# Performance work log

Measured on AMD Instinct MI355X. Metric: run time of the kernel, lower is better.

Reference implementation:

```python
import jax, jax.numpy as jnp
import numpy as np

NZ, NX, NT, NS, NR = 150, 300, 1000, 4, 400
DX, DT, FREQ = 10.0, 0.001, 15.0
# 8th-order central-difference coefficients for the 2nd derivative
C = (-205.0 / 72.0, 8.0 / 5.0, -1.0 / 5.0, 8.0 / 315.0, -1.0 / 560.0)
HALO = 4


def setup_inputs() -> dict:
    key = jax.random.key(0)
    k1, k2 = jax.random.split(key, 2)
    # velocity model in [1500, 3500] m/s
    v_map = (1500.0 + 2000.0 * jax.random.uniform(k1, (NZ, NX))).astype(jnp.float32)
    # Ricker wavelet source, slightly perturbed per shot
    t = jnp.arange(NT, dtype=jnp.float32) * DT - 1.0 / FREQ
    a = (jnp.pi * FREQ * t) ** 2
    ricker = (1.0 - 2.0 * a) * jnp.exp(-a)
    s_amp = (ricker[None, :] * (1.0 + 0.01 * jax.random.normal(k2, (NS, NT)))).astype(jnp.float32)
    # sources: shallow depth, spread in x
    sz = jnp.full((NS,), 5, dtype=jnp.int32)
    sx = jnp.round(jnp.linspace(20, NX - 21, NS)).astype(jnp.int32)
    s_loc = jnp.stack([sz, sx], axis=-1)
    # receivers: near-surface line
    rz = jnp.full((NR,), 2, dtype=jnp.int32)
    rx = jnp.round(jnp.linspace(HALO, NX - 1 - HALO, NR)).astype(jnp.int32)
    r_loc = jnp.stack([rz, rx], axis=-1)
    return {"v_map": v_map, "s_amp": s_amp, "s_loc": s_loc, "r_loc": r_loc}


def _laplacian(u, nz, nx):
    # u: [S, nz, nx]; zero-padded 8th-order 5-point-per-axis stencil
    up = jnp.pad(u, ((0, 0), (HALO, HALO), (HALO, HALO)))
    out = 2.0 * C[0] * u
    for k in range(1, 5):
        out = out + C[k] * (
            up[:, HALO + k:HALO + k + nz, HALO:HALO + nx]
            + up[:, HALO - k:HALO - k + nz, HALO:HALO + nx]
            + up[:, HALO:HALO + nz, HALO + k:HALO + k + nx]
            + up[:, HALO:HALO + nz, HALO - k:HALO - k + nx]
        )
    return out / (DX * DX)


def reference(v_map, s_amp, s_loc, r_loc):
    nz, nx = v_map.shape
    ns = s_amp.shape[0]
    sz, sx = s_loc[:, 0], s_loc[:, 1]
    rz, rx = r_loc[:, 0], r_loc[:, 1]
    shot_ids = jnp.arange(ns)
    v2dt2 = (v_map * DT) ** 2                      # [nz, nx]
    src_scale = v2dt2[sz, sx]                      # [ns]

    def step(carry, amp_t):
        u_prev, u_cur = carry                      # each [ns, nz, nx]
        u_next = 2.0 * u_cur - u_prev + v2dt2[None] * _laplacian(u_cur, nz, nx)
        u_next = u_next.at[shot_ids, sz, sx].add(src_scale * amp_t)
        rec = u_next[:, rz, rx]                    # [ns, n_rec]
        return (u_cur, u_next), rec

    u0 = jnp.zeros((ns, nz, nx), dtype=v_map.dtype)
    _, recs = jax.lax.scan(step, (u0, u0), s_amp.T)  # recs: [nt, ns, n_rec]
    rec_gth = jnp.transpose(recs, (1, 0, 2))         # [ns, nt, n_rec]
    return rec_gth
```

## Files before the change

### kernel.cpp

```cpp
#include <hip/hip_runtime.h>


#define NZ_ 150
#define NX_ 300
#define NT_ 1000
#define NS_ 4
#define NR_ 400
#define KS_ 8
#define NCH_ 9
#define NBND_ 8
#define HW_ 32
#define ZW_ 168
#define LROWS_ 98
#define BUF_ (LROWS_*ZW_)
#define THR_ 512
#define NRND_ 125
#define HELE_ 4800
#define NBATCH 19

typedef float f4 __attribute__((ext_vector_type(4)));
typedef unsigned long long u64;

__device__ __forceinline__ void astore64(u64* p, u64 v) {
    __hip_atomic_store(p, v, __ATOMIC_RELAXED, __HIP_MEMORY_SCOPE_AGENT);
}
__device__ __forceinline__ int aload32(const int* p) {
    return __hip_atomic_load(p, __ATOMIC_RELAXED, __HIP_MEMORY_SCOPE_AGENT);
}
__device__ __forceinline__ void astore32(int* p, int v) {
    __hip_atomic_store(p, v, __ATOMIC_RELAXED, __HIP_MEMORY_SCOPE_AGENT);
}
__device__ __forceinline__ void ld2_issue(u64& d, const u64* p) {
    asm volatile("global_load_dwordx2 %0, %1, off sc0 sc1" : "=v"(d) : "v"(p));
}

__global__ __launch_bounds__(THR_) void wave_tb8b(
    const float* __restrict__ v_map, const float* __restrict__ s_amp,
    const int* __restrict__ s_loc, const int* __restrict__ r_loc,
    float* __restrict__ out, int* __restrict__ flags, u64* __restrict__ halo)
{
    extern __shared__ float smem[];
    const int bi = blockIdx.x;
    const int s = bi & 3;
    const int h = bi >> 2;
    const int tid = threadIdx.x;

    const int w  = 33 + (h < 3 ? 1 : 0);
    const int x0 = 33 * h + (h < 3 ? h : 3);
    const int rhi = HW_ + w;

    for (int i = tid; i < 2 * BUF_; i += THR_) smem[i] = 0.0f;

    const int zg = tid % 38;
    const int xp = tid / 38;
    const bool comp = (tid < 494);
    const int c0 = 4 + 4 * zg;
    const int rbase = 8 * xp;

    f4 v2r[8];
#pragma unroll
    for (int i = 0; i < 8; ++i) {
        f4 vv = {0.f, 0.f, 0.f, 0.f};
        const int row = rbase + i;
        const int x = x0 - HW_ + row;
        if (comp && x >= 0 && x < NX_) {
#pragma unroll
            for (int j = 0; j < 4; ++j) {
                const int z = min(4 * zg + j, NZ_ - 1);
                const float v = v_map[z * NX_ + x] * 0.001f;
                vv[j] = v * v * 0.01f;
            }
        }
        v2r[i] = vv;
    }

    const int sz = s_loc[2 * s], sx = s_loc[2 * s + 1];
    float sS = v_map[sz * NX_ + sx] * 0.001f; sS = sS * sS;
    const int srow = sx - x0 + HW_;
    const int szg = sz >> 2;
    const int scol = 4 + sz;

    bool rown = false; int rrow = 0, rcol = 0;
    if (tid < NR_) {
        const int rz = r_loc[2 * tid];
        const int rx = r_loc[2 * tid + 1];
        if (rx >= x0 && rx < x0 + w) { rown = true; rrow = HW_ + rx - x0; rcol = 4 + rz; }
    }

    __syncthreads();

    for (int r = 0; r < NRND_; ++r) {
        for (int k = 1; k <= KS_; ++k) {
            const int tau = KS_ * r + k;
            const int ext = 4 * (KS_ - k);
            const int L  = (h == 0)        ? HW_ : HW_ - ext;
            const int R  = (h == NCH_ - 1) ? rhi : rhi + ext;
            const float* cur = smem + ((tau + 1) & 1) * BUF_;
            float*       nxt = smem + (tau & 1) * BUF_;

            if (comp && rbase < R && rbase + 8 > L) {
                f4 W[9];
#pragma unroll
                for (int q = 0; q < 8; ++q) {
                    int rr = rbase - 4 + q; rr = rr < 0 ? 0 : rr;
                    W[q] = *(const f4*)&cur[rr * ZW_ + c0];
                }
#pragma unroll
                for (int i = 0; i < 8; ++i) {
                    const int row = rbase + i;
                    const int wr = (row + 4 < LROWS_) ? (row + 4) : (LROWS_ - 1);
                    W[8] = *(const f4*)&cur[wr * ZW_ + c0];
                    if (row >= L && row < R) {
                        const f4 lf = *(const f4*)&cur[row * ZW_ + c0 - 4];
                        const f4 rt = *(const f4*)&cur[row * ZW_ + c0 + 4];
                        const f4 pv = *(const f4*)&nxt[row * ZW_ + c0];
                        float xw[12];
#pragma unroll
                        for (int j = 0; j < 4; ++j) { xw[j] = lf[j]; xw[4 + j] = W[4][j]; xw[8 + j] = rt[j]; }
                        f4 res;
#pragma unroll
                        for (int j = 0; j < 4; ++j) {
                            const float ct = xw[4 + j];
                            float lap = 2.0f * (-205.0f / 72.0f) * ct;
                            lap += (8.0f / 5.0f)    * ((xw[j + 3] + xw[j + 5]) + (W[3][j] + W[5][j]));
                            lap += (-1.0f / 5.0f)   * ((xw[j + 2] + xw[j + 6]) + (W[2][j] + W[6][j]));
                            lap += (8.0f / 315.0f)  * ((xw[j + 1] + xw[j + 7]) + (W[1][j] + W[7][j]));
                            lap += (-1.0f / 560.0f) * ((xw[j + 0] + xw[j + 8]) + (W[0][j] + W[8][j]));
                            res[j] = 2.0f * ct - pv[j] + v2r[i][j] * lap;
                        }
                        if (zg != 37) {
                            *(f4*)&nxt[row * ZW_ + c0] = res;
                        } else {
                            nxt[row * ZW_ + c0]     = res[0];
                            nxt[row * ZW_ + c0 + 1] = res[1];
                        }
                        if (row == srow && zg == szg)
                            nxt[row * ZW_ + scol] += sS * s_amp[s * NT_ + tau - 1];
                    }
#pragma unroll
                    for (int q = 0; q < 8; ++q) W[q] = W[q + 1];
                }
            }
            __syncthreads();
            if (rown) {
                const float* nb = smem + (tau & 1) * BUF_;
                out[((size_t)s * NT_ + (tau - 1)) * NR_ + tid] = nb[rrow * ZW_ + rcol];
            }
        }

        if (r < NRND_ - 1) {
            const int par = r & 1;
            if (tid < 256) {
                if (h > 0) {
                    u64* dst = halo + (size_t)(((s * NBND_ + h - 1) * 2 + 1) * 2 + par) * HELE_;
                    for (int e = tid; e < HELE_; e += 256) {
                        const int f = e / 2400, rem = e - f * 2400, row = rem / 75, zp = rem - row * 75;
                        astore64(dst + e, *(const u64*)&smem[f * BUF_ + (HW_ + row) * ZW_ + 4 + 2 * zp]);
                    }
                }
            } else {
                if (h < NCH_ - 1) {
                    u64* dst = halo + (size_t)(((s * NBND_ + h) * 2 + 0) * 2 + par) * HELE_;
                    for (int e = tid - 256; e < HELE_; e += 256) {
                        const int f = e / 2400, rem = e - f * 2400, row = rem / 75, zp = rem - row * 75;
                        astore64(dst + e, *(const u64*)&smem[f * BUF_ + (w + row) * ZW_ + 4 + 2 * zp]);
                    }
                }
            }
            asm volatile("s_waitcnt vmcnt(0)" ::: "memory");
            __syncthreads();
            if (tid == 0) {
                if (h > 0)
                    astore32(&flags[(s * NBND_ + h - 1) * 2 + 1], r + 1);
                if (h < NCH_ - 1)
                    astore32(&flags[(s * NBND_ + h) * 2 + 0], r + 1);
            }
            if (tid < 256) {
                if (h > 0) {
                    const int* fp = &flags[(s * NBND_ + h - 1) * 2 + 0];
                    while (aload32(fp) <= r) __builtin_amdgcn_s_sleep(1);
                    const u64* src = halo + (size_t)(((s * NBND_ + h - 1) * 2 + 0) * 2 + par) * HELE_;
                    u64 vb[NBATCH];
#pragma unroll
                    for (int q = 0; q < NBATCH; ++q) {
                        const int e = tid + 256 * q;
                        ld2_issue(vb[q], src + (e < HELE_ ? e : HELE_ - 1));
                    }
                    asm volatile("s_waitcnt vmcnt(0)" ::: "memory");
                    __builtin_amdgcn_sched_barrier(0);
#pragma unroll
                    for (int q = 0; q < NBATCH; ++q) {
                        const int e = tid + 256 * q;
                        if (e < HELE_) {
                            const int f = e / 2400, rem = e - f * 2400, row = rem / 75, zp = rem - row * 75;
                            *(u64*)&smem[f * BUF_ + row * ZW_ + 4 + 2 * zp] = vb[q];
                        }
                    }
                }
            } else {
                if (h < NCH_ - 1) {
                    const int* fp = &flags[(s * NBND_ + h) * 2 + 1];
                    while (aload32(fp) <= r) __builtin_amdgcn_s_sleep(1);
                    const u64* src = halo + (size_t)(((s * NBND_ + h) * 2 + 1) * 2 + par) * HELE_;
                    u64 vb[NBATCH];
#pragma unroll
                    for (int q = 0; q < NBATCH; ++q) {
                        const int e = (tid - 256) + 256 * q;
                        ld2_issue(vb[q], src + (e < HELE_ ? e : HELE_ - 1));
                    }
                    asm volatile("s_waitcnt vmcnt(0)" ::: "memory");
                    __builtin_amdgcn_sched_barrier(0);
#pragma unroll
                    for (int q = 0; q < NBATCH; ++q) {
                        const int e = (tid - 256) + 256 * q;
                        if (e < HELE_) {
                            const int f = e / 2400, rem = e - f * 2400, row = rem / 75, zp = rem - row * 75;
                            *(u64*)&smem[f * BUF_ + (rhi + row) * ZW_ + 4 + 2 * zp] = vb[q];
                        }
                    }
                }
            }
            __syncthreads();
        }
    }
}

extern "C" void kernel_launch(void* const* d_in, const int* in_sizes, int n_in,
                              void* d_out, int out_size, void* d_ws, size_t ws_size,
                              hipStream_t stream) {
    const float* v_map = (const float*)d_in[0];
    const float* s_amp = (const float*)d_in[1];
    const int*   s_loc = (const int*)d_in[2];
    const int*   r_loc = (const int*)d_in[3];
    float* out = (float*)d_out;

    int* flags = (int*)d_ws;
    u64* halo  = (u64*)((char*)d_ws + 1024);

    hipMemsetAsync(d_ws, 0, 1024, stream);

    const int smem_bytes = 2 * BUF_ * 4;
    static bool attr_set = false;
    if (!attr_set) {
        hipFuncSetAttribute((const void*)wave_tb8b,
                            hipFuncAttributeMaxDynamicSharedMemorySize, smem_bytes);
        attr_set = true;
    }

    wave_tb8b<<<dim3(NS_ * NCH_), dim3(THR_), smem_bytes, stream>>>(
        v_map, s_amp, s_loc, r_loc, out, flags, halo);
}
```

Baseline: 2.819 ms.

## Keep previous wavefield in registers and widen per-thread tile to 8x7

Each thread now computes an 8-deep z by 7-row x tile, so 266 of 320 threads are active instead of 494 of 512. The previous time level is kept in registers (pA/pB) instead of being reread from shared memory, and is refreshed from shared memory for halo rows after each exchange. The source injection is folded into the register result, and the shared row pitch shrinks to 164. The aim is fewer LDS loads per output and better reuse of the sliding window, at the cost of more registers per thread and fewer threads to hide latency.

```diff
diff --git a/kernel.cpp b/kernel.cpp
--- a/kernel.cpp
+++ b/kernel.cpp
@@ -10,13 +10,13 @@
 #define NCH_ 9
 #define NBND_ 8
 #define HW_ 32
-#define ZW_ 168
+#define ZW_ 164
 #define LROWS_ 98
 #define BUF_ (LROWS_*ZW_)
-#define THR_ 512
+#define THR_ 320
 #define NRND_ 125
 #define HELE_ 4800
-#define NBATCH 19
+#define NBATCH 30
 
 typedef float f4 __attribute__((ext_vector_type(4)));
 typedef unsigned long long u64;
@@ -34,7 +34,7 @@
     asm volatile("global_load_dwordx2 %0, %1, off sc0 sc1" : "=v"(d) : "v"(p));
 }
 
-__global__ __launch_bounds__(THR_) void wave_tb8b(
+__global__ __launch_bounds__(THR_) void wave_rp(
     const float* __restrict__ v_map, const float* __restrict__ s_amp,
     const int* __restrict__ s_loc, const int* __restrict__ r_loc,
     float* __restrict__ out, int* __restrict__ flags, u64* __restrict__ halo)
@@ -45,178 +45,214 @@
     const int h = bi >> 2;
     const int tid = threadIdx.x;
 
-    const int w  = 33 + (h < 3 ? 1 : 0);
-    const int x0 = 33 * h + (h < 3 ? h : 3);
+    const int w   = 33 + (h < 3 ? 1 : 0);
+    const int x0  = 33*h + (h < 3 ? h : 3);
     const int rhi = HW_ + w;
 
-    for (int i = tid; i < 2 * BUF_; i += THR_) smem[i] = 0.0f;
-
-    const int zg = tid % 38;
-    const int xp = tid / 38;
-    const bool comp = (tid < 494);
-    const int c0 = 4 + 4 * zg;
-    const int rbase = 8 * xp;
-
-    f4 v2r[8];
-#pragma unroll
-    for (int i = 0; i < 8; ++i) {
-        f4 vv = {0.f, 0.f, 0.f, 0.f};
+    for (int i = tid; i < 2*BUF_; i += THR_) smem[i] = 0.0f;
+
+    const int zg = tid % 19;
+    const int xp = tid / 19;
+    const bool comp = (tid < 266);
+    const int c0 = 4 + 8*zg;
+    const int rbase = 7*xp;
+
+    f4 v2A[7], v2B[7];
+#pragma unroll
+    for (int i = 0; i < 7; ++i) {
+        f4 a = {0.f,0.f,0.f,0.f}, b = {0.f,0.f,0.f,0.f};
         const int row = rbase + i;
         const int x = x0 - HW_ + row;
         if (comp && x >= 0 && x < NX_) {
 #pragma unroll
-            for (int j = 0; j < 4; ++j) {
-                const int z = min(4 * zg + j, NZ_ - 1);
-                const float v = v_map[z * NX_ + x] * 0.001f;
-                vv[j] = v * v * 0.01f;
-            }
-        }
-        v2r[i] = vv;
-    }
-
-    const int sz = s_loc[2 * s], sx = s_loc[2 * s + 1];
-    float sS = v_map[sz * NX_ + sx] * 0.001f; sS = sS * sS;
+            for (int j = 0; j < 8; ++j) {
+                const int z = 8*zg + j;
+                float val = 0.0f;
+                if (z < NZ_) { const float v = v_map[z*NX_ + x]*0.001f; val = v*v*0.01f; }
+                if (j < 4) a[j] = val; else b[j-4] = val;
+            }
+        }
+        v2A[i] = a; v2B[i] = b;
+    }
+
+    const int sz = s_loc[2*s], sx = s_loc[2*s+1];
+    float sS = v_map[sz*NX_+sx]*0.001f; sS *= sS;
     const int srow = sx - x0 + HW_;
-    const int szg = sz >> 2;
-    const int scol = 4 + sz;
-
-    bool rown = false; int rrow = 0, rcol = 0;
-    if (tid < NR_) {
-        const int rz = r_loc[2 * tid];
-        const int rx = r_loc[2 * tid + 1];
-        if (rx >= x0 && rx < x0 + w) { rown = true; rrow = HW_ + rx - x0; rcol = 4 + rz; }
-    }
+    const bool hasS = comp && (zg == (sz >> 3)) && (srow >= rbase) && (srow < rbase+7);
+    const int sel = sz & 7;
+
+    int nrec = 0; int rI[2], rRow[2], rCol[2];
+#pragma unroll
+    for (int q = 0; q < 2; ++q) {
+        const int rr = tid + q*THR_;
+        if (rr < NR_) {
+            const int rz = r_loc[2*rr], rx = r_loc[2*rr+1];
+            if (rx >= x0 && rx < x0+w) { rI[nrec]=rr; rRow[nrec]=HW_+rx-x0; rCol[nrec]=4+rz; ++nrec; }
+        }
+    }
+
+    f4 pA[7], pB[7];
+#pragma unroll
+    for (int i = 0; i < 7; ++i) { pA[i] = f4{0.f,0.f,0.f,0.f}; pB[i] = f4{0.f,0.f,0.f,0.f}; }
 
     __syncthreads();
 
     for (int r = 0; r < NRND_; ++r) {
         for (int k = 1; k <= KS_; ++k) {
-            const int tau = KS_ * r + k;
-            const int ext = 4 * (KS_ - k);
-            const int L  = (h == 0)        ? HW_ : HW_ - ext;
-            const int R  = (h == NCH_ - 1) ? rhi : rhi + ext;
-            const float* cur = smem + ((tau + 1) & 1) * BUF_;
-            float*       nxt = smem + (tau & 1) * BUF_;
-
-            if (comp && rbase < R && rbase + 8 > L) {
-                f4 W[9];
+            const int tau = KS_*r + k;
+            const int ext = 4*(KS_-k);
+            const int L = (h==0)        ? HW_ : HW_-ext;
+            const int R = (h==NCH_-1)   ? rhi : rhi+ext;
+            const float* cur = smem + ((tau+1)&1)*BUF_;
+            float*       nxt = smem + (tau&1)*BUF_;
+            const float amp = s_amp[s*NT_ + tau - 1];
+
+            if (comp && rbase < R && rbase+7 > L) {
+                f4 WA[9], WB[9];
 #pragma unroll
                 for (int q = 0; q < 8; ++q) {
-                    int rr = rbase - 4 + q; rr = rr < 0 ? 0 : rr;
-                    W[q] = *(const f4*)&cur[rr * ZW_ + c0];
-                }
-#pragma unroll
-                for (int i = 0; i < 8; ++i) {
-                    const int row = rbase + i;
-                    const int wr = (row + 4 < LROWS_) ? (row + 4) : (LROWS_ - 1);
-                    W[8] = *(const f4*)&cur[wr * ZW_ + c0];
+                    int rr = rbase-4+q; rr = rr < 0 ? 0 : rr;
+                    WA[q] = *(const f4*)&cur[rr*ZW_ + c0];
+                    WB[q] = *(const f4*)&cur[rr*ZW_ + c0+4];
+                }
+#pragma unroll
+                for (int i = 0; i < 7; ++i) {
+                    const int row = rbase+i;
+                    const int wr = (row+4 < LROWS_) ? row+4 : LROWS_-1;
+                    WA[8] = *(const f4*)&cur[wr*ZW_ + c0];
+                    WB[8] = *(const f4*)&cur[wr*ZW_ + c0+4];
                     if (row >= L && row < R) {
-                        const f4 lf = *(const f4*)&cur[row * ZW_ + c0 - 4];
-                        const f4 rt = *(const f4*)&cur[row * ZW_ + c0 + 4];
-                        const f4 pv = *(const f4*)&nxt[row * ZW_ + c0];
-                        float xw[12];
-#pragma unroll
-                        for (int j = 0; j < 4; ++j) { xw[j] = lf[j]; xw[4 + j] = W[4][j]; xw[8 + j] = rt[j]; }
-                        f4 res;
+                        const f4 lf = *(const f4*)&cur[row*ZW_ + c0-4];
+                        const f4 rt = *(const f4*)&cur[row*ZW_ + c0+8];
+                        float xw[16];
 #pragma unroll
                         for (int j = 0; j < 4; ++j) {
-                            const float ct = xw[4 + j];
-                            float lap = 2.0f * (-205.0f / 72.0f) * ct;
-                            lap += (8.0f / 5.0f)    * ((xw[j + 3] + xw[j + 5]) + (W[3][j] + W[5][j]));
-                            lap += (-1.0f / 5.0f)   * ((xw[j + 2] + xw[j + 6]) + (W[2][j] + W[6][j]));
-                            lap += (8.0f / 315.0f)  * ((xw[j + 1] + xw[j + 7]) + (W[1][j] + W[7][j]));
-                            lap += (-1.0f / 560.0f) * ((xw[j + 0] + xw[j + 8]) + (W[0][j] + W[8][j]));
-                            res[j] = 2.0f * ct - pv[j] + v2r[i][j] * lap;
-                        }
-                        if (zg != 37) {
-                            *(f4*)&nxt[row * ZW_ + c0] = res;
-                        } else {
-                            nxt[row * ZW_ + c0]     = res[0];
-                            nxt[row * ZW_ + c0 + 1] = res[1];
-                        }
-                        if (row == srow && zg == szg)
-                            nxt[row * ZW_ + scol] += sS * s_amp[s * NT_ + tau - 1];
-                    }
-#pragma unroll
-                    for (int q = 0; q < 8; ++q) W[q] = W[q + 1];
-                }
-            }
-            __syncthreads();
-            if (rown) {
-                const float* nb = smem + (tau & 1) * BUF_;
-                out[((size_t)s * NT_ + (tau - 1)) * NR_ + tid] = nb[rrow * ZW_ + rcol];
-            }
-        }
-
-        if (r < NRND_ - 1) {
+                            xw[j] = lf[j]; xw[4+j] = WA[4][j]; xw[8+j] = WB[4][j]; xw[12+j] = rt[j];
+                        }
+                        f4 rA, rB;
+#pragma unroll
+                        for (int j = 0; j < 4; ++j) {
+                            const float ct = xw[4+j];
+                            float lap = 2.0f*(-205.0f/72.0f)*ct;
+                            lap += (8.0f/5.0f)   *((xw[j+3]+xw[j+5])  + (WA[3][j]+WA[5][j]));
+                            lap += (-1.0f/5.0f)  *((xw[j+2]+xw[j+6])  + (WA[2][j]+WA[6][j]));
+                            lap += (8.0f/315.0f) *((xw[j+1]+xw[j+7])  + (WA[1][j]+WA[7][j]));
+                            lap += (-1.0f/560.0f)*((xw[j+0]+xw[j+8])  + (WA[0][j]+WA[8][j]));
+                            rA[j] = 2.0f*ct - pA[i][j] + v2A[i][j]*lap;
+                        }
+#pragma unroll
+                        for (int j = 0; j < 4; ++j) {
+                            const float ct = xw[8+j];
+                            float lap = 2.0f*(-205.0f/72.0f)*ct;
+                            lap += (8.0f/5.0f)   *((xw[j+7]+xw[j+9])  + (WB[3][j]+WB[5][j]));
+                            lap += (-1.0f/5.0f)  *((xw[j+6]+xw[j+10]) + (WB[2][j]+WB[6][j]));
+                            lap += (8.0f/315.0f) *((xw[j+5]+xw[j+11]) + (WB[1][j]+WB[7][j]));
+                            lap += (-1.0f/560.0f)*((xw[j+4]+xw[j+12]) + (WB[0][j]+WB[8][j]));
+                            rB[j] = 2.0f*ct - pB[i][j] + v2B[i][j]*lap;
+                        }
+                        if (hasS && row == srow) {
+                            const float add = sS*amp;
+#pragma unroll
+                            for (int j = 0; j < 4; ++j) {
+                                if (sel == j)   rA[j] += add;
+                                if (sel == 4+j) rB[j] += add;
+                            }
+                        }
+                        *(f4*)&nxt[row*ZW_ + c0]   = rA;
+                        *(f4*)&nxt[row*ZW_ + c0+4] = rB;
+                    }
+                    pA[i] = WA[4]; pB[i] = WB[4];
+#pragma unroll
+                    for (int q = 0; q < 8; ++q) { WA[q] = WA[q+1]; WB[q] = WB[q+1]; }
+                }
+            }
+            __syncthreads();
+            if (nrec) {
+                const float* nb = smem + (tau&1)*BUF_;
+                out[((size_t)s*NT_+(tau-1))*NR_ + rI[0]] = nb[rRow[0]*ZW_ + rCol[0]];
+                if (nrec > 1)
+                    out[((size_t)s*NT_+(tau-1))*NR_ + rI[1]] = nb[rRow[1]*ZW_ + rCol[1]];
+            }
+        }
+
+        if (r < NRND_-1) {
             const int par = r & 1;
-            if (tid < 256) {
+            if (tid < 160) {
                 if (h > 0) {
-                    u64* dst = halo + (size_t)(((s * NBND_ + h - 1) * 2 + 1) * 2 + par) * HELE_;
-                    for (int e = tid; e < HELE_; e += 256) {
-                        const int f = e / 2400, rem = e - f * 2400, row = rem / 75, zp = rem - row * 75;
-                        astore64(dst + e, *(const u64*)&smem[f * BUF_ + (HW_ + row) * ZW_ + 4 + 2 * zp]);
+                    u64* dst = halo + (size_t)(((s*NBND_ + h-1)*2 + 1)*2 + par)*HELE_;
+                    for (int e = tid; e < HELE_; e += 160) {
+                        const int f = e/2400, rem = e - f*2400, row = rem/75, zp = rem - row*75;
+                        astore64(dst + e, *(const u64*)&smem[f*BUF_ + (HW_+row)*ZW_ + 4 + 2*zp]);
                     }
                 }
             } else {
-                if (h < NCH_ - 1) {
-                    u64* dst = halo + (size_t)(((s * NBND_ + h) * 2 + 0) * 2 + par) * HELE_;
-                    for (int e = tid - 256; e < HELE_; e += 256) {
-                        const int f = e / 2400, rem = e - f * 2400, row = rem / 75, zp = rem - row * 75;
-                        astore64(dst + e, *(const u64*)&smem[f * BUF_ + (w + row) * ZW_ + 4 + 2 * zp]);
+                if (h < NCH_-1) {
+                    u64* dst = halo + (size_t)(((s*NBND_ + h)*2 + 0)*2 + par)*HELE_;
+                    for (int e = tid-160; e < HELE_; e += 160) {
+                        const int f = e/2400, rem = e - f*2400, row = rem/75, zp = rem - row*75;
+                        astore64(dst + e, *(const u64*)&smem[f*BUF_ + (w+row)*ZW_ + 4 + 2*zp]);
                     }
                 }
             }
             asm volatile("s_waitcnt vmcnt(0)" ::: "memory");
             __syncthreads();
             if (tid == 0) {
-                if (h > 0)
-                    astore32(&flags[(s * NBND_ + h - 1) * 2 + 1], r + 1);
-                if (h < NCH_ - 1)
-                    astore32(&flags[(s * NBND_ + h) * 2 + 0], r + 1);
-            }
-            if (tid < 256) {
+                if (h > 0)      astore32(&flags[(s*NBND_ + h-1)*2 + 1], r+1);
+                if (h < NCH_-1) astore32(&flags[(s*NBND_ + h)*2 + 0], r+1);
+            }
+            if (tid < 160) {
                 if (h > 0) {
-                    const int* fp = &flags[(s * NBND_ + h - 1) * 2 + 0];
+                    const int* fp = &flags[(s*NBND_ + h-1)*2 + 0];
                     while (aload32(fp) <= r) __builtin_amdgcn_s_sleep(1);
-                    const u64* src = halo + (size_t)(((s * NBND_ + h - 1) * 2 + 0) * 2 + par) * HELE_;
+                    const u64* src = halo + (size_t)(((s*NBND_ + h-1)*2 + 0)*2 + par)*HELE_;
                     u64 vb[NBATCH];
 #pragma unroll
                     for (int q = 0; q < NBATCH; ++q) {
-                        const int e = tid + 256 * q;
-                        ld2_issue(vb[q], src + (e < HELE_ ? e : HELE_ - 1));
+                        const int e = tid + 160*q;
+                        ld2_issue(vb[q], src + (e < HELE_ ? e : HELE_-1));
                     }
                     asm volatile("s_waitcnt vmcnt(0)" ::: "memory");
                     __builtin_amdgcn_sched_barrier(0);
 #pragma unroll
                     for (int q = 0; q < NBATCH; ++q) {
-                        const int e = tid + 256 * q;
+                        const int e = tid + 160*q;
                         if (e < HELE_) {
-                            const int f = e / 2400, rem = e - f * 2400, row = rem / 75, zp = rem - row * 75;
-                            *(u64*)&smem[f * BUF_ + row * ZW_ + 4 + 2 * zp] = vb[q];
+                            const int f = e/2400, rem = e - f*2400, row = rem/75, zp = rem - row*75;
+                            *(u64*)&smem[f*BUF_ + row*ZW_ + 4 + 2*zp] = vb[q];
                         }
                     }
                 }
             } else {
-                if (h < NCH_ - 1) {
-                    const int* fp = &flags[(s * NBND_ + h) * 2 + 1];
+                if (h < NCH_-1) {
+                    const int* fp = &flags[(s*NBND_ + h)*2 + 1];
                     while (aload32(fp) <= r) __builtin_amdgcn_s_sleep(1);
-                    const u64* src = halo + (size_t)(((s * NBND_ + h) * 2 + 1) * 2 + par) * HELE_;
+                    const u64* src = halo + (size_t)(((s*NBND_ + h)*2 + 1)*2 + par)*HELE_;
                     u64 vb[NBATCH];
 #pragma unroll
                     for (int q = 0; q < NBATCH; ++q) {
-                        const int e = (tid - 256) + 256 * q;
-                        ld2_issue(vb[q], src + (e < HELE_ ? e : HELE_ - 1));
+                        const int e = (tid-160) + 160*q;
+                        ld2_issue(vb[q], src + (e < HELE_ ? e : HELE_-1));
                     }
                     asm volatile("s_waitcnt vmcnt(0)" ::: "memory");
                     __builtin_amdgcn_sched_barrier(0);
 #pragma unroll
                     for (int q = 0; q < NBATCH; ++q) {
-                        const int e = (tid - 256) + 256 * q;
+                        const int e = (tid-160) + 160*q;
                         if (e < HELE_) {
-                            const int f = e / 2400, rem = e - f * 2400, row = rem / 75, zp = rem - row * 75;
-                            *(u64*)&smem[f * BUF_ + (rhi + row) * ZW_ + 4 + 2 * zp] = vb[q];
-                        }
+                            const int f = e/2400, rem = e - f*2400, row = rem/75, zp = rem - row*75;
+                            *(u64*)&smem[f*BUF_ + (rhi+row)*ZW_ + 4 + 2*zp] = vb[q];
+                        }
+                    }
+                }
+            }
+            __syncthreads();
+            if (comp) {
+#pragma unroll
+                for (int i = 0; i < 7; ++i) {
+                    const int row = rbase + i;
+                    if (row < HW_ || row >= rhi) {
+                        pA[i] = *(const f4*)&smem[BUF_ + row*ZW_ + c0];
+                        pB[i] = *(const f4*)&smem[BUF_ + row*ZW_ + c0+4];
                     }
                 }
             }
@@ -242,11 +278,11 @@
     const int smem_bytes = 2 * BUF_ * 4;
     static bool attr_set = false;
     if (!attr_set) {
-        hipFuncSetAttribute((const void*)wave_tb8b,
+        hipFuncSetAttribute((const void*)wave_rp,
                             hipFuncAttributeMaxDynamicSharedMemorySize, smem_bytes);
         attr_set = true;
     }
 
-    wave_tb8b<<<dim3(NS_ * NCH_), dim3(THR_), smem_bytes, stream>>>(
+    wave_rp<<<dim3(NS_ * NCH_), dim3(THR_), smem_bytes, stream>>>(
         v_map, s_amp, s_loc, r_loc, out, flags, halo);
 }
```

New measurement: 4.586 ms. 62.7% more time.

## Overlap halo exchange with interior stencil of next round's first step

Applied to the files above, without the earlier changes.

Splits each round's first time step into an interior part, computed while waiting for the neighbour halo flags, and a boundary part computed after the halo arrives. It also sends one of the two halo time levels early, after step 7, so less data is written in the serialized exchange. The aim is to hide inter-block synchronization latency behind useful compute. In exchange it adds an extra barrier and a split stencil pass, plus more complex row-range logic.

```diff
diff --git a/kernel.cpp b/kernel.cpp
--- a/kernel.cpp
+++ b/kernel.cpp
@@ -34,7 +34,61 @@
     asm volatile("global_load_dwordx2 %0, %1, off sc0 sc1" : "=v"(d) : "v"(p));
 }
 
-__global__ __launch_bounds__(THR_) void wave_tb8b(
+__device__ __forceinline__ void fd_step(
+    float* __restrict__ smem, const int cb, const int nb,
+    const int lo1, const int hi1, const int lo2, const int hi2,
+    const bool comp, const int rbase, const int c0, const int zg, const f4* v2r,
+    const int srow, const int szg, const int scol, const float srcadd)
+{
+    if (!comp) return;
+    if (!((rbase < hi1 && rbase + 8 > lo1) || (rbase < hi2 && rbase + 8 > lo2))) return;
+    const float* cur = smem + cb;
+    float*       nxt = smem + nb;
+    f4 W[9];
+#pragma unroll
+    for (int q = 0; q < 8; ++q) {
+        int rr = rbase - 4 + q; rr = rr < 0 ? 0 : rr;
+        W[q] = *(const f4*)&cur[rr * ZW_ + c0];
+    }
+#pragma unroll
+    for (int i = 0; i < 8; ++i) {
+        const int row = rbase + i;
+        const int wr = (row + 4 < LROWS_) ? (row + 4) : (LROWS_ - 1);
+        W[8] = *(const f4*)&cur[wr * ZW_ + c0];
+        const bool act = (row >= lo1 && row < hi1) || (row >= lo2 && row < hi2);
+        if (act) {
+            const f4 lf = *(const f4*)&cur[row * ZW_ + c0 - 4];
+            const f4 rt = *(const f4*)&cur[row * ZW_ + c0 + 4];
+            const f4 pv = *(const f4*)&nxt[row * ZW_ + c0];
+            float xw[12];
+#pragma unroll
+            for (int j = 0; j < 4; ++j) { xw[j] = lf[j]; xw[4 + j] = W[4][j]; xw[8 + j] = rt[j]; }
+            f4 res;
+#pragma unroll
+            for (int j = 0; j < 4; ++j) {
+                const float ct = xw[4 + j];
+                float lap = 2.0f * (-205.0f / 72.0f) * ct;
+                lap += (8.0f / 5.0f)    * ((xw[j + 3] + xw[j + 5]) + (W[3][j] + W[5][j]));
+                lap += (-1.0f / 5.0f)   * ((xw[j + 2] + xw[j + 6]) + (W[2][j] + W[6][j]));
+                lap += (8.0f / 315.0f)  * ((xw[j + 1] + xw[j + 7]) + (W[1][j] + W[7][j]));
+                lap += (-1.0f / 560.0f) * ((xw[j + 0] + xw[j + 8]) + (W[0][j] + W[8][j]));
+                res[j] = 2.0f * ct - pv[j] + v2r[i][j] * lap;
+            }
+            if (zg != 37) {
+                *(f4*)&nxt[row * ZW_ + c0] = res;
+            } else {
+                nxt[row * ZW_ + c0]     = res[0];
+                nxt[row * ZW_ + c0 + 1] = res[1];
+            }
+            if (row == srow && zg == szg)
+                nxt[row * ZW_ + scol] += srcadd;
+        }
+#pragma unroll
+        for (int q = 0; q < 8; ++q) W[q] = W[q + 1];
+    }
+}
+
+__global__ __launch_bounds__(THR_) void wave_ov(
     const float* __restrict__ v_map, const float* __restrict__ s_amp,
     const int* __restrict__ s_loc, const int* __restrict__ r_loc,
     float* __restrict__ out, int* __restrict__ flags, u64* __restrict__ halo)
@@ -87,61 +141,42 @@
         if (rx >= x0 && rx < x0 + w) { rown = true; rrow = HW_ + rx - x0; rcol = 4 + rz; }
     }
 
+    const int L1 = (h == 0)        ? HW_ : HW_ - 28;
+    const int R1 = (h == NCH_ - 1) ? rhi : rhi + 28;
+
     __syncthreads();
 
     for (int r = 0; r < NRND_; ++r) {
-        for (int k = 1; k <= KS_; ++k) {
+        const int kstart = (r == 0) ? 1 : 2;
+        for (int k = kstart; k <= KS_; ++k) {
             const int tau = KS_ * r + k;
             const int ext = 4 * (KS_ - k);
             const int L  = (h == 0)        ? HW_ : HW_ - ext;
             const int R  = (h == NCH_ - 1) ? rhi : rhi + ext;
-            const float* cur = smem + ((tau + 1) & 1) * BUF_;
-            float*       nxt = smem + (tau & 1) * BUF_;
-
-            if (comp && rbase < R && rbase + 8 > L) {
-                f4 W[9];
-#pragma unroll
-                for (int q = 0; q < 8; ++q) {
-                    int rr = rbase - 4 + q; rr = rr < 0 ? 0 : rr;
-                    W[q] = *(const f4*)&cur[rr * ZW_ + c0];
-                }
-#pragma unroll
-                for (int i = 0; i < 8; ++i) {
-                    const int row = rbase + i;
-                    const int wr = (row + 4 < LROWS_) ? (row + 4) : (LROWS_ - 1);
-                    W[8] = *(const f4*)&cur[wr * ZW_ + c0];
-                    if (row >= L && row < R) {
-                        const f4 lf = *(const f4*)&cur[row * ZW_ + c0 - 4];
-                        const f4 rt = *(const f4*)&cur[row * ZW_ + c0 + 4];
-                        const f4 pv = *(const f4*)&nxt[row * ZW_ + c0];
-                        float xw[12];
-#pragma unroll
-                        for (int j = 0; j < 4; ++j) { xw[j] = lf[j]; xw[4 + j] = W[4][j]; xw[8 + j] = rt[j]; }
-                        f4 res;
-#pragma unroll
-                        for (int j = 0; j < 4; ++j) {
-                            const float ct = xw[4 + j];
-                            float lap = 2.0f * (-205.0f / 72.0f) * ct;
-                            lap += (8.0f / 5.0f)    * ((xw[j + 3] + xw[j + 5]) + (W[3][j] + W[5][j]));
-                            lap += (-1.0f / 5.0f)   * ((xw[j + 2] + xw[j + 6]) + (W[2][j] + W[6][j]));
-                            lap += (8.0f / 315.0f)  * ((xw[j + 1] + xw[j + 7]) + (W[1][j] + W[7][j]));
-                            lap += (-1.0f / 560.0f) * ((xw[j + 0] + xw[j + 8]) + (W[0][j] + W[8][j]));
-                            res[j] = 2.0f * ct - pv[j] + v2r[i][j] * lap;
-                        }
-                        if (zg != 37) {
-                            *(f4*)&nxt[row * ZW_ + c0] = res;
-                        } else {
-                            nxt[row * ZW_ + c0]     = res[0];
-                            nxt[row * ZW_ + c0 + 1] = res[1];
-                        }
-                        if (row == srow && zg == szg)
-                            nxt[row * ZW_ + scol] += sS * s_amp[s * NT_ + tau - 1];
-                    }
-#pragma unroll
-                    for (int q = 0; q < 8; ++q) W[q] = W[q + 1];
-                }
-            }
-            __syncthreads();
+            fd_step(smem, ((tau + 1) & 1) * BUF_, (tau & 1) * BUF_,
+                    L, R, 0, 0, comp, rbase, c0, zg, v2r,
+                    srow, szg, scol, sS * s_amp[s * NT_ + tau - 1]);
+            __syncthreads();
+            if (k == 7 && r < NRND_ - 1) {
+                const int par = r & 1;
+                if (tid < 256) {
+                    if (h > 0) {
+                        u64* dst = halo + (size_t)(((s * NBND_ + h - 1) * 2 + 1) * 2 + par) * HELE_;
+                        for (int e = tid; e < 2400; e += 256) {
+                            const int row = e / 75, zp = e - row * 75;
+                            astore64(dst + 2400 + e, *(const u64*)&smem[BUF_ + (HW_ + row) * ZW_ + 4 + 2 * zp]);
+                        }
+                    }
+                } else {
+                    if (h < NCH_ - 1) {
+                        u64* dst = halo + (size_t)(((s * NBND_ + h) * 2 + 0) * 2 + par) * HELE_;
+                        for (int e = tid - 256; e < 2400; e += 256) {
+                            const int row = e / 75, zp = e - row * 75;
+                            astore64(dst + 2400 + e, *(const u64*)&smem[BUF_ + (w + row) * ZW_ + 4 + 2 * zp]);
+                        }
+                    }
+                }
+            }
             if (rown) {
                 const float* nb = smem + (tau & 1) * BUF_;
                 out[((size_t)s * NT_ + (tau - 1)) * NR_ + tid] = nb[rrow * ZW_ + rcol];
@@ -150,31 +185,33 @@
 
         if (r < NRND_ - 1) {
             const int par = r & 1;
+            const int tau1 = KS_ * (r + 1) + 1;
             if (tid < 256) {
                 if (h > 0) {
                     u64* dst = halo + (size_t)(((s * NBND_ + h - 1) * 2 + 1) * 2 + par) * HELE_;
-                    for (int e = tid; e < HELE_; e += 256) {
-                        const int f = e / 2400, rem = e - f * 2400, row = rem / 75, zp = rem - row * 75;
-                        astore64(dst + e, *(const u64*)&smem[f * BUF_ + (HW_ + row) * ZW_ + 4 + 2 * zp]);
+                    for (int e = tid; e < 2400; e += 256) {
+                        const int row = e / 75, zp = e - row * 75;
+                        astore64(dst + e, *(const u64*)&smem[(HW_ + row) * ZW_ + 4 + 2 * zp]);
                     }
                 }
             } else {
                 if (h < NCH_ - 1) {
                     u64* dst = halo + (size_t)(((s * NBND_ + h) * 2 + 0) * 2 + par) * HELE_;
-                    for (int e = tid - 256; e < HELE_; e += 256) {
-                        const int f = e / 2400, rem = e - f * 2400, row = rem / 75, zp = rem - row * 75;
-                        astore64(dst + e, *(const u64*)&smem[f * BUF_ + (w + row) * ZW_ + 4 + 2 * zp]);
+                    for (int e = tid - 256; e < 2400; e += 256) {
+                        const int row = e / 75, zp = e - row * 75;
+                        astore64(dst + e, *(const u64*)&smem[(w + row) * ZW_ + 4 + 2 * zp]);
                     }
                 }
             }
             asm volatile("s_waitcnt vmcnt(0)" ::: "memory");
             __syncthreads();
             if (tid == 0) {
-                if (h > 0)
-                    astore32(&flags[(s * NBND_ + h - 1) * 2 + 1], r + 1);
-                if (h < NCH_ - 1)
-                    astore32(&flags[(s * NBND_ + h) * 2 + 0], r + 1);
-            }
+                if (h > 0)      astore32(&flags[(s * NBND_ + h - 1) * 2 + 1], r + 1);
+                if (h < NCH_ - 1) astore32(&flags[(s * NBND_ + h) * 2 + 0], r + 1);
+            }
+            fd_step(smem, 0 , BUF_ ,
+                    HW_ + 4, rhi - 4, 0, 0, comp, rbase, c0, zg, v2r,
+                    srow, szg, scol, sS * s_amp[s * NT_ + tau1 - 1]);
             if (tid < 256) {
                 if (h > 0) {
                     const int* fp = &flags[(s * NBND_ + h - 1) * 2 + 0];
@@ -221,6 +258,12 @@
                 }
             }
             __syncthreads();
+            fd_step(smem, 0, BUF_, L1, HW_ + 4, rhi - 4, R1,
+                    comp, rbase, c0, zg, v2r,
+                    srow, szg, scol, sS * s_amp[s * NT_ + tau1 - 1]);
+            __syncthreads();
+            if (rown)
+                out[((size_t)s * NT_ + (tau1 - 1)) * NR_ + tid] = smem[BUF_ + rrow * ZW_ + rcol];
         }
     }
 }
@@ -242,11 +285,11 @@
     const int smem_bytes = 2 * BUF_ * 4;
     static bool attr_set = false;
     if (!attr_set) {
-        hipFuncSetAttribute((const void*)wave_tb8b,
+        hipFuncSetAttribute((const void*)wave_ov,
                             hipFuncAttributeMaxDynamicSharedMemorySize, smem_bytes);
         attr_set = true;
     }
 
-    wave_tb8b<<<dim3(NS_ * NCH_), dim3(THR_), smem_bytes, stream>>>(
+    wave_ov<<<dim3(NS_ * NCH_), dim3(THR_), smem_bytes, stream>>>(
         v_map, s_amp, s_loc, r_loc, out, flags, halo);
 }
```

Result: slower. 2.913 ms (+3.3%).

## Split domain into 18 narrower chunks with shared global strip halo exchange

Applied to the files above, without the earlier changes.

Doubles the number of x-chunks per shot from 9 to 18 so more blocks run concurrently, shrinking each block's local buffer and per-thread row count. Halo exchange moves from paired neighbour buffers to a shared per-shot global strip where each block publishes its owned columns and consumers wait on flags for every chunk overlapping their 32-column halo. The aim is a shorter per-round critical path, in exchange for more redundant halo computation per owned column and more flag polling.

```diff
diff --git a/kernel.cpp b/kernel.cpp
--- a/kernel.cpp
+++ b/kernel.cpp
@@ -7,15 +7,14 @@
 #define NS_ 4
 #define NR_ 400
 #define KS_ 8
-#define NCH_ 9
-#define NBND_ 8
+#define NCH_ 18
 #define HW_ 32
 #define ZW_ 168
-#define LROWS_ 98
+#define LROWS_ 81
 #define BUF_ (LROWS_*ZW_)
 #define THR_ 512
 #define NRND_ 125
-#define HELE_ 4800
+#define SLAB_ (300*75)
 #define NBATCH 19
 
 typedef float f4 __attribute__((ext_vector_type(4)));
@@ -33,11 +32,14 @@
 __device__ __forceinline__ void ld2_issue(u64& d, const u64* p) {
     asm volatile("global_load_dwordx2 %0, %1, off sc0 sc1" : "=v"(d) : "v"(p));
 }
-
-__global__ __launch_bounds__(THR_) void wave_tb8b(
+__device__ __forceinline__ int chunk_of(int x) {
+    return x < 204 ? x / 17 : 12 + (x - 204) / 16;
+}
+
+__global__ __launch_bounds__(THR_) void wave_st(
     const float* __restrict__ v_map, const float* __restrict__ s_amp,
     const int* __restrict__ s_loc, const int* __restrict__ r_loc,
-    float* __restrict__ out, int* __restrict__ flags, u64* __restrict__ halo)
+    float* __restrict__ out, int* __restrict__ flags, u64* __restrict__ strip)
 {
     extern __shared__ float smem[];
     const int bi = blockIdx.x;
@@ -45,21 +47,22 @@
     const int h = bi >> 2;
     const int tid = threadIdx.x;
 
-    const int w  = 33 + (h < 3 ? 1 : 0);
-    const int x0 = 33 * h + (h < 3 ? h : 3);
+    const int w  = (h < 12) ? 17 : 16;
+    const int x0 = (h < 12) ? 17 * h : 204 + 16 * (h - 12);
+    const int x1 = x0 + w;
     const int rhi = HW_ + w;
 
     for (int i = tid; i < 2 * BUF_; i += THR_) smem[i] = 0.0f;
 
     const int zg = tid % 38;
     const int xp = tid / 38;
-    const bool comp = (tid < 494);
+    const bool comp = (tid < 418);
     const int c0 = 4 + 4 * zg;
-    const int rbase = 8 * xp;
-
-    f4 v2r[8];
-#pragma unroll
-    for (int i = 0; i < 8; ++i) {
+    const int rbase = 7 * xp;
+
+    f4 v2r[7];
+#pragma unroll
+    for (int i = 0; i < 7; ++i) {
         f4 vv = {0.f, 0.f, 0.f, 0.f};
         const int row = rbase + i;
         const int x = x0 - HW_ + row;
@@ -84,8 +87,13 @@
     if (tid < NR_) {
         const int rz = r_loc[2 * tid];
         const int rx = r_loc[2 * tid + 1];
-        if (rx >= x0 && rx < x0 + w) { rown = true; rrow = HW_ + rx - x0; rcol = 4 + rz; }
-    }
+        if (rx >= x0 && rx < x1) { rown = true; rrow = HW_ + rx - x0; rcol = 4 + rz; }
+    }
+
+    const int nL = min(32, x0);
+    const int nR = min(32, NX_ - x1);
+    const int gL = (h > 0) ? chunk_of(x0 - nL) : 0;
+    const int gR = (h < NCH_ - 1) ? chunk_of(x1 + nR - 1) : 0;
 
     __syncthreads();
 
@@ -93,12 +101,12 @@
         for (int k = 1; k <= KS_; ++k) {
             const int tau = KS_ * r + k;
             const int ext = 4 * (KS_ - k);
-            const int L  = (h == 0)        ? HW_ : HW_ - ext;
-            const int R  = (h == NCH_ - 1) ? rhi : rhi + ext;
+            const int L  = HW_ - min(ext, x0);
+            const int R  = rhi + min(ext, NX_ - x1);
             const float* cur = smem + ((tau + 1) & 1) * BUF_;
             float*       nxt = smem + (tau & 1) * BUF_;
 
-            if (comp && rbase < R && rbase + 8 > L) {
+            if (comp && rbase < R && rbase + 7 > L) {
                 f4 W[9];
 #pragma unroll
                 for (int q = 0; q < 8; ++q) {
@@ -106,7 +114,7 @@
                     W[q] = *(const f4*)&cur[rr * ZW_ + c0];
                 }
 #pragma unroll
-                for (int i = 0; i < 8; ++i) {
+                for (int i = 0; i < 7; ++i) {
                     const int row = rbase + i;
                     const int wr = (row + 4 < LROWS_) ? (row + 4) : (LROWS_ - 1);
                     W[8] = *(const f4*)&cur[wr * ZW_ + c0];
@@ -150,72 +158,82 @@
 
         if (r < NRND_ - 1) {
             const int par = r & 1;
-            if (tid < 256) {
-                if (h > 0) {
-                    u64* dst = halo + (size_t)(((s * NBND_ + h - 1) * 2 + 1) * 2 + par) * HELE_;
-                    for (int e = tid; e < HELE_; e += 256) {
-                        const int f = e / 2400, rem = e - f * 2400, row = rem / 75, zp = rem - row * 75;
-                        astore64(dst + e, *(const u64*)&smem[f * BUF_ + (HW_ + row) * ZW_ + 4 + 2 * zp]);
-                    }
-                }
-            } else {
-                if (h < NCH_ - 1) {
-                    u64* dst = halo + (size_t)(((s * NBND_ + h) * 2 + 0) * 2 + par) * HELE_;
-                    for (int e = tid - 256; e < HELE_; e += 256) {
-                        const int f = e / 2400, rem = e - f * 2400, row = rem / 75, zp = rem - row * 75;
-                        astore64(dst + e, *(const u64*)&smem[f * BUF_ + (w + row) * ZW_ + 4 + 2 * zp]);
+            u64* sp = strip + (size_t)((s * 2 + par) * 2) * SLAB_;
+            {
+                const int w75 = w * 75, E2 = 2 * w75;
+#pragma unroll
+                for (int q = 0; q < 5; ++q) {
+                    const int e = tid + 512 * q;
+                    if (e < E2) {
+                        const int f = (e >= w75);
+                        const int rem = e - f * w75;
+                        const int col = rem / 75, zp = rem - col * 75;
+                        astore64(sp + (size_t)f * SLAB_ + (x0 + col) * 75 + zp,
+                                 *(const u64*)&smem[f * BUF_ + (HW_ + col) * ZW_ + 4 + 2 * zp]);
                     }
                 }
             }
             asm volatile("s_waitcnt vmcnt(0)" ::: "memory");
             __syncthreads();
-            if (tid == 0) {
-                if (h > 0)
-                    astore32(&flags[(s * NBND_ + h - 1) * 2 + 1], r + 1);
-                if (h < NCH_ - 1)
-                    astore32(&flags[(s * NBND_ + h) * 2 + 0], r + 1);
-            }
+            if (tid == 0) astore32(&flags[s * NCH_ + h], r + 1);
             if (tid < 256) {
-                if (h > 0) {
-                    const int* fp = &flags[(s * NBND_ + h - 1) * 2 + 0];
-                    while (aload32(fp) <= r) __builtin_amdgcn_s_sleep(1);
-                    const u64* src = halo + (size_t)(((s * NBND_ + h - 1) * 2 + 0) * 2 + par) * HELE_;
+                if (h > 0 && nL > 0) {
+                    for (int g = gL; g < h; ++g) {
+                        const int* fp = &flags[s * NCH_ + g];
+                        while (aload32(fp) <= r) __builtin_amdgcn_s_sleep(1);
+                    }
+                    const int n75 = nL * 75, E = 2 * n75;
                     u64 vb[NBATCH];
 #pragma unroll
                     for (int q = 0; q < NBATCH; ++q) {
                         const int e = tid + 256 * q;
-                        ld2_issue(vb[q], src + (e < HELE_ ? e : HELE_ - 1));
+                        const int ec = (e < E) ? e : 0;
+                        const int f = (ec >= n75);
+                        const int rem = ec - f * n75;
+                        const int col = rem / 75, zp = rem - col * 75;
+                        ld2_issue(vb[q], sp + (size_t)f * SLAB_ + (x0 - nL + col) * 75 + zp);
                     }
                     asm volatile("s_waitcnt vmcnt(0)" ::: "memory");
                     __builtin_amdgcn_sched_barrier(0);
 #pragma unroll
                     for (int q = 0; q < NBATCH; ++q) {
                         const int e = tid + 256 * q;
-                        if (e < HELE_) {
-                            const int f = e / 2400, rem = e - f * 2400, row = rem / 75, zp = rem - row * 75;
-                            *(u64*)&smem[f * BUF_ + row * ZW_ + 4 + 2 * zp] = vb[q];
+                        if (e < E) {
+                            const int f = (e >= n75);
+                            const int rem = e - f * n75;
+                            const int col = rem / 75, zp = rem - col * 75;
+                            *(u64*)&smem[f * BUF_ + (HW_ - nL + col) * ZW_ + 4 + 2 * zp] = vb[q];
                         }
                     }
                 }
             } else {
-                if (h < NCH_ - 1) {
-                    const int* fp = &flags[(s * NBND_ + h) * 2 + 1];
-                    while (aload32(fp) <= r) __builtin_amdgcn_s_sleep(1);
-                    const u64* src = halo + (size_t)(((s * NBND_ + h) * 2 + 1) * 2 + par) * HELE_;
+                if (h < NCH_ - 1 && nR > 0) {
+                    for (int g = h + 1; g <= gR; ++g) {
+                        const int* fp = &flags[s * NCH_ + g];
+                        while (aload32(fp) <= r) __builtin_amdgcn_s_sleep(1);
+                    }
+                    const int tidS = tid - 256;
+                    const int n75 = nR * 75, E = 2 * n75;
                     u64 vb[NBATCH];
 #pragma unroll
                     for (int q = 0; q < NBATCH; ++q) {
-                        const int e = (tid - 256) + 256 * q;
-                        ld2_issue(vb[q], src + (e < HELE_ ? e : HELE_ - 1));
+                        const int e = tidS + 256 * q;
+                        const int ec = (e < E) ? e : 0;
+                        const int f = (ec >= n75);
+                        const int rem = ec - f * n75;
+                        const int col = rem / 75, zp = rem - col * 75;
+                        ld2_issue(vb[q], sp + (size_t)f * SLAB_ + (x1 + col) * 75 + zp);
                     }
                     asm volatile("s_waitcnt vmcnt(0)" ::: "memory");
                     __builtin_amdgcn_sched_barrier(0);
 #pragma unroll
                     for (int q = 0; q < NBATCH; ++q) {
-                        const int e = (tid - 256) + 256 * q;
-                        if (e < HELE_) {
-                            const int f = e / 2400, rem = e - f * 2400, row = rem / 75, zp = rem - row * 75;
-                            *(u64*)&smem[f * BUF_ + (rhi + row) * ZW_ + 4 + 2 * zp] = vb[q];
+                        const int e = tidS + 256 * q;
+                        if (e < E) {
+                            const int f = (e >= n75);
+                            const int rem = e - f * n75;
+                            const int col = rem / 75, zp = rem - col * 75;
+                            *(u64*)&smem[f * BUF_ + (rhi + col) * ZW_ + 4 + 2 * zp] = vb[q];
                         }
                     }
                 }
@@ -235,18 +253,18 @@
     float* out = (float*)d_out;
 
     int* flags = (int*)d_ws;
-    u64* halo  = (u64*)((char*)d_ws + 1024);
+    u64* strip = (u64*)((char*)d_ws + 1024);
 
     hipMemsetAsync(d_ws, 0, 1024, stream);
 
     const int smem_bytes = 2 * BUF_ * 4;
     static bool attr_set = false;
     if (!attr_set) {
-        hipFuncSetAttribute((const void*)wave_tb8b,
+        hipFuncSetAttribute((const void*)wave_st,
                             hipFuncAttributeMaxDynamicSharedMemorySize, smem_bytes);
         attr_set = true;
     }
 
-    wave_tb8b<<<dim3(NS_ * NCH_), dim3(THR_), smem_bytes, stream>>>(
-        v_map, s_amp, s_loc, r_loc, out, flags, halo);
-}
+    wave_st<<<dim3(NS_ * NCH_), dim3(THR_), smem_bytes, stream>>>(
+        v_map, s_amp, s_loc, r_loc, out, flags, strip);
+}
```

New measurement: 3.490 ms. 1.24x slower.
